# Performance work log

Hardware: AMD Instinct MI355X
Metric: run time of the kernel (lower is better)

The kernel has to match this reference:

```python
import jax, jax.numpy as jnp
import numpy as np

TEMPERATURE = 0.07
EPS = 1e-8  # torch F.cosine_similarity eps


def reference(features):
    B, F, D = features.shape
    x = features.reshape(B * F, D)  # [N, D]
    # cosine similarity = normalized-dot; torch clamps norm at eps
    norm = jnp.maximum(jnp.linalg.norm(x, axis=-1, keepdims=True), EPS)
    xn = x / norm
    logits = (xn @ xn.T) / TEMPERATURE  # [N, N]
    # cross_entropy with labels = arange(N): mean(logsumexp - diagonal)
    lse = jax.scipy.special.logsumexp(logits, axis=-1)
    diag = jnp.diagonal(logits)
    return jnp.mean(lse - diag)


def setup_inputs() -> dict:
    key = jax.random.key(0)
    features = jax.random.normal(key, (512, 16, 512), dtype=jnp.float32)
    return {"features": features}
```

## Files before the change

### kernel.cpp

```cpp
#include <hip/hip_runtime.h>
#include <hip/hip_bf16.h>
#include <cstdint>

#define N_TOT 8192
#define DDIM  512
#define DBYTES 512
#define NBLK  64
#define NTRI  (NBLK * (NBLK + 1) / 2)
constexpr float INV_T = 1.0f / 0.07f;

typedef uint8_t u8;
typedef __attribute__((ext_vector_type(8))) int i32x8_t;
typedef __attribute__((ext_vector_type(4))) float f32x4_t;


__device__ __forceinline__ void load16_to_lds(const void* g, void* l) {
  __builtin_amdgcn_global_load_lds(
      (const __attribute__((address_space(1))) unsigned int*)g,
      (__attribute__((address_space(3))) unsigned int*)l, 16, 0, 0);
}

__global__ __launch_bounds__(256) void normalize_kernel(const float* __restrict__ X,
                                                        u8* __restrict__ Xn,
                                                        float* __restrict__ tsum,
                                                        float* __restrict__ out) {
  if (blockIdx.x < 32) tsum[blockIdx.x * 256 + threadIdx.x] = 0.0f;
  if (blockIdx.x == 32 && threadIdx.x == 0) out[0] = 0.0f;
  const int lane = threadIdx.x & 63;
  const int row  = blockIdx.x * 4 + (threadIdx.x >> 6);
  const float4* xr = (const float4*)(X + (size_t)row * DDIM);
  float4 v0 = xr[lane];
  float4 v1 = xr[lane + 64];
  float s = v0.x * v0.x + v0.y * v0.y + v0.z * v0.z + v0.w * v0.w
          + v1.x * v1.x + v1.y * v1.y + v1.z * v1.z + v1.w * v1.w;
#pragma unroll
  for (int m = 1; m < 64; m <<= 1) s += __shfl_xor(s, m);
  const float scale = 1.0f / fmaxf(sqrtf(s), 1e-8f);
  int w0 = __builtin_amdgcn_cvt_pk_fp8_f32(v0.x * scale, v0.y * scale, 0, 0);
  w0     = __builtin_amdgcn_cvt_pk_fp8_f32(v0.z * scale, v0.w * scale, w0, 1);
  int w1 = __builtin_amdgcn_cvt_pk_fp8_f32(v1.x * scale, v1.y * scale, 0, 0);
  w1     = __builtin_amdgcn_cvt_pk_fp8_f32(v1.z * scale, v1.w * scale, w1, 1);
  uint32_t* orow = (uint32_t*)(Xn + (size_t)row * DBYTES);
  orow[lane]      = (uint32_t)w0;
  orow[lane + 64] = (uint32_t)w1;
}

__global__ __launch_bounds__(256, 2) void gemm_exp_rowsum(const u8* __restrict__ Xn,
                                                          float* __restrict__ tsum) {
  __shared__ __align__(16) u8 sA[128 * 256];
  __shared__ __align__(16) u8 sB[128 * 256];

  const int k = blockIdx.x;
  int bi = (int)((sqrtf(8.0f * (float)k + 1.0f) - 1.0f) * 0.5f);
  while ((bi + 1) * (bi + 2) / 2 <= k) ++bi;
  while (bi * (bi + 1) / 2 > k) --bi;
  const int bj = k - bi * (bi + 1) / 2;
  const int rowBase = bi * 128;
  const int colBase = bj * 128;
  const bool isDiag = (bi == bj);

  const int t    = threadIdx.x;
  const int lane = t & 63;
  const int l15  = lane & 15;
  const int quad = lane >> 4;
  const int w    = t >> 6;
  const int wm   = w >> 1;
  const int wn   = w & 1;

  f32x4_t acc[4][4];
#pragma unroll
  for (int i = 0; i < 4; i++)
#pragma unroll
    for (int j = 0; j < 4; j++) acc[i][j] = {0.f, 0.f, 0.f, 0.f};

  const int srow = t >> 4;
  const int jj   = t & 15;
  const int jl   = (jj & 8) | ((jj & 7) ^ (srow & 7));
  const u8* gA = Xn + (size_t)(rowBase + srow) * DBYTES + jl * 16;
  const u8* gB = Xn + (size_t)(colBase + srow) * DBYTES + jl * 16;
  u8* lA = sA + t * 16;
  u8* lB = sB + t * 16;

  for (int k0 = 0; k0 < DBYTES; k0 += 256) {
#pragma unroll
    for (int i = 0; i < 8; i++) {
      load16_to_lds(gA + (size_t)(i * 16) * DBYTES + k0, lA + i * 4096);
      load16_to_lds(gB + (size_t)(i * 16) * DBYTES + k0, lB + i * 4096);
    }
    __syncthreads();

#pragma unroll
    for (int kk = 0; kk < 2; kk++) {
      i32x8_t a[4], b[4];
#pragma unroll
      for (int mi = 0; mi < 4; mi++) {
        const int row = wm * 64 + mi * 16 + l15;
        const int s0 = row * 256 + (kk * 8 + ((quad * 2) ^ (row & 7))) * 16;
        const int s1 = row * 256 + (kk * 8 + ((quad * 2 + 1) ^ (row & 7))) * 16;
        int4 lo = *(const int4*)&sA[s0];
        int4 hi = *(const int4*)&sA[s1];
        a[mi] = (i32x8_t){lo.x, lo.y, lo.z, lo.w, hi.x, hi.y, hi.z, hi.w};
      }
#pragma unroll
      for (int ni = 0; ni < 4; ni++) {
        const int row = wn * 64 + ni * 16 + l15;
        const int s0 = row * 256 + (kk * 8 + ((quad * 2) ^ (row & 7))) * 16;
        const int s1 = row * 256 + (kk * 8 + ((quad * 2 + 1) ^ (row & 7))) * 16;
        int4 lo = *(const int4*)&sB[s0];
        int4 hi = *(const int4*)&sB[s1];
        b[ni] = (i32x8_t){lo.x, lo.y, lo.z, lo.w, hi.x, hi.y, hi.z, hi.w};
      }
#pragma unroll
      for (int mi = 0; mi < 4; mi++)
#pragma unroll
        for (int ni = 0; ni < 4; ni++)
          acc[mi][ni] = __builtin_amdgcn_mfma_scale_f32_16x16x128_f8f6f4(
              a[mi], b[ni], acc[mi][ni], 0, 0, 0, 0x7F7F7F7Fu, 0, 0x7F7F7F7Fu);
    }
    __syncthreads();
  }

  if (isDiag) {
#pragma unroll
    for (int mi = 0; mi < 4; mi++) {
#pragma unroll
      for (int r = 0; r < 4; r++) {
        const int row = rowBase + wm * 64 + mi * 16 + quad * 4 + r;
        float rs = 0.0f;
#pragma unroll
        for (int ni = 0; ni < 4; ni++) {
          const int col = colBase + wn * 64 + ni * 16 + l15;
          const float e = __expf((acc[mi][ni][r] - 1.0f) * INV_T);
          rs += (row == col) ? 0.0f : e;
        }
        rs += __shfl_xor(rs, 1);
        rs += __shfl_xor(rs, 2);
        rs += __shfl_xor(rs, 4);
        rs += __shfl_xor(rs, 8);
        if (l15 == 0) atomicAdd(&tsum[row], rs);
      }
    }
  } else {
    float csum[4] = {0.f, 0.f, 0.f, 0.f};
#pragma unroll
    for (int mi = 0; mi < 4; mi++) {
#pragma unroll
      for (int r = 0; r < 4; r++) {
        const int row = rowBase + wm * 64 + mi * 16 + quad * 4 + r;
        float rs = 0.0f;
#pragma unroll
        for (int ni = 0; ni < 4; ni++) {
          const float e = __expf((acc[mi][ni][r] - 1.0f) * INV_T);
          rs += e;
          csum[ni] += e;
        }
        rs += __shfl_xor(rs, 1);
        rs += __shfl_xor(rs, 2);
        rs += __shfl_xor(rs, 4);
        rs += __shfl_xor(rs, 8);
        if (l15 == 0) atomicAdd(&tsum[row], rs);
      }
    }
#pragma unroll
    for (int ni = 0; ni < 4; ni++) {
      csum[ni] += __shfl_xor(csum[ni], 16);
      csum[ni] += __shfl_xor(csum[ni], 32);
      if (quad == 0) atomicAdd(&tsum[colBase + wn * 64 + ni * 16 + l15], csum[ni]);
    }
  }
}

__global__ __launch_bounds__(256) void finalize_kernel(const float* __restrict__ tsum,
                                                       float* __restrict__ out) {
  const int i = blockIdx.x * 256 + threadIdx.x;
  float s = log1pf(tsum[i]);
#pragma unroll
  for (int m = 1; m < 64; m <<= 1) s += __shfl_xor(s, m);
  __shared__ float ws[4];
  if ((threadIdx.x & 63) == 0) ws[threadIdx.x >> 6] = s;
  __syncthreads();
  if (threadIdx.x == 0)
    atomicAdd(out, (ws[0] + ws[1] + ws[2] + ws[3]) * (1.0f / N_TOT));
}

extern "C" void kernel_launch(void* const* d_in, const int* in_sizes, int n_in,
                              void* d_out, int out_size, void* d_ws, size_t ws_size,
                              hipStream_t stream) {
  const float* X = (const float*)d_in[0];
  float* out = (float*)d_out;

  float* tsum = (float*)d_ws;
  u8* Xn = (u8*)d_ws + 65536;

  normalize_kernel<<<N_TOT / 4, 256, 0, stream>>>(X, Xn, tsum, out);
  gemm_exp_rowsum<<<NTRI, 256, 0, stream>>>(Xn, tsum);
  finalize_kernel<<<N_TOT / 256, 256, 0, stream>>>(tsum, out);
}
```

Before: 121.7 us.

## Add dedicated producer wave with double-buffered LDS and flag-based sync

Adds a fifth wavefront that acts as a loader. It streams the K dimension in 128-byte chunks into double-buffered LDS and signals readiness through workgroup-scope atomic flags, replacing the block-wide barriers. Compute waves spin on the flags, copy fragments into registers, and then signal buffer release, so the next load overlaps the MFMA work. This removes the __syncthreads stalls and lets loads and compute overlap. The cost is spin-wait overhead, an extra idle-ish wave, and a change in occupancy targets (320 threads, 3 blocks).

```diff
diff --git a/kernel.cpp b/kernel.cpp
--- a/kernel.cpp
+++ b/kernel.cpp
@@ -45,10 +45,12 @@
   orow[lane + 64] = (uint32_t)w1;
 }
 
-__global__ __launch_bounds__(256, 2) void gemm_exp_rowsum(const u8* __restrict__ Xn,
+__global__ __launch_bounds__(320, 3) void gemm_exp_rowsum(const u8* __restrict__ Xn,
                                                           float* __restrict__ tsum) {
-  __shared__ __align__(16) u8 sA[128 * 256];
-  __shared__ __align__(16) u8 sB[128 * 256];
+  __shared__ __align__(16) u8 sA[2][128 * 128];
+  __shared__ __align__(16) u8 sB[2][128 * 128];
+  __shared__ int flagv[4];
+  __shared__ int donev[4];
 
   const int k = blockIdx.x;
   int bi = (int)((sqrtf(8.0f * (float)k + 1.0f) - 1.0f) * 0.5f);
@@ -61,9 +63,39 @@
 
   const int t    = threadIdx.x;
   const int lane = t & 63;
+  const int w    = t >> 6;
+
+  if (t < 4) { flagv[t] = 0; donev[t] = 0; }
+  __syncthreads();
+
+  if (w == 4) {
+    const int rl = lane >> 3;
+    const int jl = (lane & 7) ^ (rl & 7);
+    const u8* pA = Xn + (size_t)(rowBase + rl) * DBYTES + jl * 16;
+    const u8* pB = Xn + (size_t)(colBase + rl) * DBYTES + jl * 16;
+    for (int it = 0; it < 4; ++it) {
+      if (it >= 2) {
+        while (__hip_atomic_load(&donev[it - 2], __ATOMIC_ACQUIRE,
+                                 __HIP_MEMORY_SCOPE_WORKGROUP) < 4) {}
+      }
+      u8* dA = sA[it & 1];
+      u8* dB = sB[it & 1];
+      const int k0 = it * 128;
+#pragma unroll
+      for (int i = 0; i < 16; i++)
+        load16_to_lds(pA + (size_t)(i * 8) * DBYTES + k0, dA + i * 1024 + lane * 16);
+#pragma unroll
+      for (int i = 0; i < 16; i++)
+        load16_to_lds(pB + (size_t)(i * 8) * DBYTES + k0, dB + i * 1024 + lane * 16);
+      __builtin_amdgcn_s_waitcnt(0);
+      __hip_atomic_store(&flagv[it], 1, __ATOMIC_RELEASE,
+                         __HIP_MEMORY_SCOPE_WORKGROUP);
+    }
+    return;
+  }
+
   const int l15  = lane & 15;
   const int quad = lane >> 4;
-  const int w    = t >> 6;
   const int wm   = w >> 1;
   const int wn   = w & 1;
 
@@ -73,51 +105,41 @@
 #pragma unroll
     for (int j = 0; j < 4; j++) acc[i][j] = {0.f, 0.f, 0.f, 0.f};
 
-  const int srow = t >> 4;
-  const int jj   = t & 15;
-  const int jl   = (jj & 8) | ((jj & 7) ^ (srow & 7));
-  const u8* gA = Xn + (size_t)(rowBase + srow) * DBYTES + jl * 16;
-  const u8* gB = Xn + (size_t)(colBase + srow) * DBYTES + jl * 16;
-  u8* lA = sA + t * 16;
-  u8* lB = sB + t * 16;
-
-  for (int k0 = 0; k0 < DBYTES; k0 += 256) {
-#pragma unroll
-    for (int i = 0; i < 8; i++) {
-      load16_to_lds(gA + (size_t)(i * 16) * DBYTES + k0, lA + i * 4096);
-      load16_to_lds(gB + (size_t)(i * 16) * DBYTES + k0, lB + i * 4096);
-    }
-    __syncthreads();
-
-#pragma unroll
-    for (int kk = 0; kk < 2; kk++) {
-      i32x8_t a[4], b[4];
-#pragma unroll
-      for (int mi = 0; mi < 4; mi++) {
-        const int row = wm * 64 + mi * 16 + l15;
-        const int s0 = row * 256 + (kk * 8 + ((quad * 2) ^ (row & 7))) * 16;
-        const int s1 = row * 256 + (kk * 8 + ((quad * 2 + 1) ^ (row & 7))) * 16;
-        int4 lo = *(const int4*)&sA[s0];
-        int4 hi = *(const int4*)&sA[s1];
-        a[mi] = (i32x8_t){lo.x, lo.y, lo.z, lo.w, hi.x, hi.y, hi.z, hi.w};
-      }
-#pragma unroll
-      for (int ni = 0; ni < 4; ni++) {
-        const int row = wn * 64 + ni * 16 + l15;
-        const int s0 = row * 256 + (kk * 8 + ((quad * 2) ^ (row & 7))) * 16;
-        const int s1 = row * 256 + (kk * 8 + ((quad * 2 + 1) ^ (row & 7))) * 16;
-        int4 lo = *(const int4*)&sB[s0];
-        int4 hi = *(const int4*)&sB[s1];
-        b[ni] = (i32x8_t){lo.x, lo.y, lo.z, lo.w, hi.x, hi.y, hi.z, hi.w};
-      }
-#pragma unroll
-      for (int mi = 0; mi < 4; mi++)
-#pragma unroll
-        for (int ni = 0; ni < 4; ni++)
-          acc[mi][ni] = __builtin_amdgcn_mfma_scale_f32_16x16x128_f8f6f4(
-              a[mi], b[ni], acc[mi][ni], 0, 0, 0, 0x7F7F7F7Fu, 0, 0x7F7F7F7Fu);
-    }
-    __syncthreads();
+  for (int it = 0; it < 4; ++it) {
+    while (__hip_atomic_load(&flagv[it], __ATOMIC_ACQUIRE,
+                             __HIP_MEMORY_SCOPE_WORKGROUP) == 0) {}
+    const u8* bufA = sA[it & 1];
+    const u8* bufB = sB[it & 1];
+
+    i32x8_t a[4], b[4];
+#pragma unroll
+    for (int mi = 0; mi < 4; mi++) {
+      const int row = wm * 64 + mi * 16 + l15;
+      const int s0 = (((quad * 2) ^ (row & 7)) * 16);
+      const int s1 = (((quad * 2 + 1) ^ (row & 7)) * 16);
+      int4 lo = *(const int4*)&bufA[row * 128 + s0];
+      int4 hi = *(const int4*)&bufA[row * 128 + s1];
+      a[mi] = (i32x8_t){lo.x, lo.y, lo.z, lo.w, hi.x, hi.y, hi.z, hi.w};
+    }
+#pragma unroll
+    for (int ni = 0; ni < 4; ni++) {
+      const int row = wn * 64 + ni * 16 + l15;
+      const int s0 = (((quad * 2) ^ (row & 7)) * 16);
+      const int s1 = (((quad * 2 + 1) ^ (row & 7)) * 16);
+      int4 lo = *(const int4*)&bufB[row * 128 + s0];
+      int4 hi = *(const int4*)&bufB[row * 128 + s1];
+      b[ni] = (i32x8_t){lo.x, lo.y, lo.z, lo.w, hi.x, hi.y, hi.z, hi.w};
+    }
+
+    __hip_atomic_fetch_add(&donev[it], 1, __ATOMIC_RELEASE,
+                           __HIP_MEMORY_SCOPE_WORKGROUP);
+
+#pragma unroll
+    for (int mi = 0; mi < 4; mi++)
+#pragma unroll
+      for (int ni = 0; ni < 4; ni++)
+        acc[mi][ni] = __builtin_amdgcn_mfma_scale_f32_16x16x128_f8f6f4(
+            a[mi], b[ni], acc[mi][ni], 0, 0, 0, 0x7F7F7F7Fu, 0, 0x7F7F7F7Fu);
   }
 
   if (isDiag) {
@@ -193,6 +215,6 @@
   u8* Xn = (u8*)d_ws + 65536;
 
   normalize_kernel<<<N_TOT / 4, 256, 0, stream>>>(X, Xn, tsum, out);
-  gemm_exp_rowsum<<<NTRI, 256, 0, stream>>>(Xn, tsum);
+  gemm_exp_rowsum<<<NTRI, 320, 0, stream>>>(Xn, tsum);
   finalize_kernel<<<N_TOT / 256, 256, 0, stream>>>(tsum, out);
 }
```

Result: slower. 133.0 us (+9.3%).
